# Performance work log

Hardware: AMD Instinct MI355X
Metric: run time of the kernel (lower is better)

Reference implementation:

```python
import jax, jax.numpy as jnp
import numpy as np

B, D, P, C = 256, 2048, 8192, 8
N_CLUSTERS = P // C
MOMENTUM, TEMP = 0.2, 0.07
NEG_INF = jnp.float32(-1e30)


def setup_inputs() -> dict:
    key = jax.random.key(0)
    k1, k2, k3 = jax.random.split(key, 3)
    batch_feat = jax.random.normal(k1, (B, D), dtype=jnp.float32)
    batch_feat = batch_feat / jnp.linalg.norm(batch_feat, axis=1, keepdims=True)
    memory = jax.random.normal(k2, (P, D), dtype=jnp.float32)
    memory = memory / jnp.linalg.norm(memory, axis=1, keepdims=True)
    abs_proxy_label = jax.random.randint(k3, (B,), 0, P, dtype=jnp.int32)
    # each proxy is a (camera, cluster) pair: proxy p -> cam p % C, cluster p // C
    proxy_cam = (jnp.arange(P, dtype=jnp.int32) % C)
    proxy_cluster = (jnp.arange(P, dtype=jnp.int32) // C)
    camid = abs_proxy_label % C               # consistent with mapper[cam]
    pseudo_cluster_label = abs_proxy_label // C
    return dict(batch_feat=batch_feat, memory=memory,
                abs_proxy_label=abs_proxy_label, camid=camid,
                pseudo_cluster_label=pseudo_cluster_label,
                proxy_cam=proxy_cam, proxy_cluster=proxy_cluster,
                epoch=10, inter_loss_epoch=5, k=50)


def reference(batch_feat, memory, abs_proxy_label, camid, pseudo_cluster_label,
              proxy_cam, proxy_cluster, epoch, inter_loss_epoch, k):
    # ---------------- intra-camera proxy loss ----------------
    sim = (batch_feat @ memory.T) / TEMP                      # [B, P]
    cam_mask = camid[:, None] == proxy_cam[None, :]           # per-cam proxy subset
    logits = jnp.where(cam_mask, sim, NEG_INF)
    lse = jax.nn.logsumexp(logits, axis=1)
    tgt = jnp.take_along_axis(logits, abs_proxy_label[:, None].astype(jnp.int32), axis=1)[:, 0]
    ce = lse - tgt                                            # per-sample CE over its cam's proxies
    ones = jnp.ones((B,), dtype=jnp.float32)
    cam_counts = jax.ops.segment_sum(ones, camid, num_segments=C)
    ce_per_cam = jax.ops.segment_sum(ce, camid, num_segments=C)
    intra_loss = jnp.sum(jnp.where(cam_counts > 0, ce_per_cam / jnp.maximum(cam_counts, 1.0), 0.0))

    loss = intra_loss
    # ---------------- inter-camera loss ----------------
    if epoch >= inter_loss_epoch:
        sim_det = jax.lax.stop_gradient(batch_feat) @ memory.T     # kNN uses detached feat, no temp
        pos_mask = (proxy_cluster[None, :] == pseudo_cluster_label[:, None]) & \
                   (proxy_cam[None, :] != camid[:, None])          # same cluster, different cam
        neg_mask = proxy_cluster[None, :] != pseudo_cluster_label[:, None]  # inlier, different cluster
        neg_sim = jnp.where(neg_mask, sim_det, NEG_INF)
        thresh = jax.lax.top_k(neg_sim, k)[0][:, -1]               # drop k nearest negatives
        keep_neg = neg_mask & (sim_det < thresh[:, None])
        full_mask = pos_mask | keep_neg
        inter_logits = jnp.where(full_mask, sim, NEG_INF)
        logsm = inter_logits - jax.nn.logsumexp(inter_logits, axis=1, keepdims=True)
        pos_card = jnp.sum(pos_mask, axis=1).astype(jnp.float32)
        pos_sum = jnp.sum(jnp.where(pos_mask, logsm, 0.0), axis=1)
        loss_i = jnp.where(pos_card > 0, -pos_sum / jnp.maximum(pos_card, 1.0), 0.0)
        inter_per_cam = jax.ops.segment_sum(loss_i, camid, num_segments=C)
        loss = loss + jnp.sum(jnp.where(cam_counts > 0,
                                        0.5 * inter_per_cam / jnp.maximum(cam_counts, 1.0), 0.0))

    # ---------------- EMA memory-bank scatter update (torch does this in backward) ----------------
    def step(mem, xy):
        x, y = xy
        m = MOMENTUM * mem[y] + (1.0 - MOMENTUM) * x
        m = m / jnp.linalg.norm(m)
        return mem.at[y].set(m), None
    new_memory, _ = jax.lax.scan(
        step, memory, (jax.lax.stop_gradient(batch_feat), abs_proxy_label))
    return loss, new_memory
```

## Files before the change

kernel.cpp:

```cpp
#include <hip/hip_runtime.h>
#include <cstdint>

#define NB 256
#define ND 2048
#define NP 8192
#define NEG_INF_F (-1e30f)
#define INV_TEMP (1.0f/0.07f)

typedef __attribute__((ext_vector_type(8))) short          short8;
typedef __attribute__((ext_vector_type(8))) unsigned short ushort8;
typedef __attribute__((ext_vector_type(4))) float          floatx4;

__device__ __forceinline__ unsigned short f2bf(float f) {
  unsigned u = __float_as_uint(f);
  return (unsigned short)((u + 0x7fffu + ((u >> 16) & 1u)) >> 16);
}

__global__ __launch_bounds__(256)
void prep_kernel(const float* __restrict__ mem, const float* __restrict__ feat,
                 unsigned short* __restrict__ Mb, unsigned short* __restrict__ Fb,
                 float* __restrict__ memcopy ) {
  const int b = blockIdx.x, t = threadIdx.x;
  if (b < 8192) {
    const float4* src = (const float4*)(mem + (size_t)b * ND) + 2 * t;
    float4 a = src[0], c = src[1];
    ushort8 r;
    r[0]=f2bf(a.x); r[1]=f2bf(a.y); r[2]=f2bf(a.z); r[3]=f2bf(a.w);
    r[4]=f2bf(c.x); r[5]=f2bf(c.y); r[6]=f2bf(c.z); r[7]=f2bf(c.w);
    *(ushort8*)(Mb + (size_t)b * ND + 8 * t) = r;
    float* dst = memcopy + (size_t)b * ND + 8 * t;
    dst[0]=a.x; dst[1]=a.y; dst[2]=a.z; dst[3]=a.w;
    dst[4]=c.x; dst[5]=c.y; dst[6]=c.z; dst[7]=c.w;
  } else {
    const int i = (b - 8192) * 256 + t;
    const float4* src = (const float4*)feat + 2 * (size_t)i;
    float4 a = src[0], c = src[1];
    ushort8 r;
    r[0]=f2bf(a.x); r[1]=f2bf(a.y); r[2]=f2bf(a.z); r[3]=f2bf(a.w);
    r[4]=f2bf(c.x); r[5]=f2bf(c.y); r[6]=f2bf(c.z); r[7]=f2bf(c.w);
    *(ushort8*)(Fb + 8 * (size_t)i) = r;
  }
}

#define GLOAD_LDS16(g, l) __builtin_amdgcn_global_load_lds( \
  (const __attribute__((address_space(1))) unsigned int*)(g), \
  (__attribute__((address_space(3))) unsigned int*)(l), 16, 0, 0)

__global__ __launch_bounds__(256, 2)
void gemm_kernel(const unsigned short* __restrict__ Fb,
                 const unsigned short* __restrict__ Mb,
                 float* __restrict__ Sout) {
  __shared__ unsigned short sA[2][64 * 64];
  __shared__ unsigned short sB[2][128 * 64];
  const int tid  = threadIdx.x;
  const int wave = tid >> 6;
  const int lane = tid & 63;
  const int frow = lane & 15;
  const int kg   = lane >> 4;
  const int bn0  = blockIdx.x * 128;
  const int bm0  = blockIdx.y * 64;
  const size_t kofs = (size_t)blockIdx.z * 1024;

  const unsigned short* gA[2];
  #pragma unroll
  for (int q = 0; q < 2; ++q) {
    int c = q * 256 + tid, r = c >> 3, kc = (c & 7) ^ (r & 7);
    gA[q] = Fb + (size_t)(bm0 + r) * ND + kofs + kc * 8;
  }
  const unsigned short* gB[4];
  #pragma unroll
  for (int q = 0; q < 4; ++q) {
    int c = q * 256 + tid, r = c >> 3, kc = (c & 7) ^ (r & 7);
    gB[q] = Mb + (size_t)(bn0 + r) * ND + kofs + kc * 8;
  }
  const int ldsb = wave * 512;

  int offA[4][2], offB[2][2];
  #pragma unroll
  for (int m = 0; m < 4; ++m)
    #pragma unroll
    for (int kf = 0; kf < 2; ++kf) {
      int r = m * 16 + frow, sc = (kf * 4 + kg) ^ (r & 7);
      offA[m][kf] = r * 64 + sc * 8;
    }
  #pragma unroll
  for (int n = 0; n < 2; ++n)
    #pragma unroll
    for (int kf = 0; kf < 2; ++kf) {
      int r = wave * 32 + n * 16 + frow, sc = (kf * 4 + kg) ^ (r & 7);
      offB[n][kf] = r * 64 + sc * 8;
    }

  floatx4 acc[4][2];
  #pragma unroll
  for (int m = 0; m < 4; ++m)
    #pragma unroll
    for (int n = 0; n < 2; ++n)
      #pragma unroll
      for (int r = 0; r < 4; ++r) acc[m][n][r] = 0.f;

  auto stage = [&](int buf, int kt) {
    int kk = kt * 64;
    #pragma unroll
    for (int q = 0; q < 2; ++q) GLOAD_LDS16(gA[q] + kk, &sA[buf][q * 2048 + ldsb]);
    #pragma unroll
    for (int q = 0; q < 4; ++q) GLOAD_LDS16(gB[q] + kk, &sB[buf][q * 2048 + ldsb]);
  };
  auto compute = [&](int buf) {
    short8 af[4][2], bf[2][2];
    #pragma unroll
    for (int m = 0; m < 4; ++m)
      #pragma unroll
      for (int kf = 0; kf < 2; ++kf) af[m][kf] = *(const short8*)&sA[buf][offA[m][kf]];
    #pragma unroll
    for (int n = 0; n < 2; ++n)
      #pragma unroll
      for (int kf = 0; kf < 2; ++kf) bf[n][kf] = *(const short8*)&sB[buf][offB[n][kf]];
    #pragma unroll
    for (int m = 0; m < 4; ++m)
      #pragma unroll
      for (int n = 0; n < 2; ++n) {
        acc[m][n] = __builtin_amdgcn_mfma_f32_16x16x32_bf16(af[m][0], bf[n][0], acc[m][n], 0, 0, 0);
        acc[m][n] = __builtin_amdgcn_mfma_f32_16x16x32_bf16(af[m][1], bf[n][1], acc[m][n], 0, 0, 0);
      }
  };

  stage(0, 0);
  __syncthreads();
  int cur = 0;
  for (int kt = 0; kt < 15; ++kt) {
    stage(cur ^ 1, kt + 1);
    compute(cur);
    __syncthreads();
    cur ^= 1;
  }
  compute(cur);

  float* Sp = Sout + (size_t)blockIdx.z * ((size_t)NB * NP);
  #pragma unroll
  for (int m = 0; m < 4; ++m) {
    int row = bm0 + 16 * m + 4 * kg;
    #pragma unroll
    for (int n = 0; n < 2; ++n) {
      int col = bn0 + wave * 32 + 16 * n + frow;
      #pragma unroll
      for (int r = 0; r < 4; ++r)
        Sp[(size_t)(row + r) * NP + col] = acc[m][n][r];
    }
  }
}

__global__ __launch_bounds__(1024)
void row_kernel(const float* __restrict__ S,
                const int* __restrict__ label,
                const int* __restrict__ camid,
                const int* __restrict__ pcl,
                const int* __restrict__ epoch_p,
                const int* __restrict__ ilep_p,
                const int* __restrict__ k_p,
                float* __restrict__ ce_out,
                float* __restrict__ li_out) {
  __shared__ float red[2][16];
  const int i = blockIdx.x, t = threadIdx.x, w = t >> 6;
  const bool l0 = (t & 63) == 0;
  int ph = 0;

  auto bred_sum = [&](float x) -> float {
    #pragma unroll
    for (int o = 32; o; o >>= 1) x += __shfl_xor(x, o);
    if (l0) red[ph][w] = x;
    __syncthreads();
    float s = 0.f;
    #pragma unroll
    for (int q = 0; q < 16; ++q) s += red[ph][q];
    ph ^= 1;
    return s;
  };
  auto bred_max = [&](float x) -> float {
    #pragma unroll
    for (int o = 32; o; o >>= 1) x = fmaxf(x, __shfl_xor(x, o));
    if (l0) red[ph][w] = x;
    __syncthreads();
    float s = NEG_INF_F;
    #pragma unroll
    for (int q = 0; q < 16; ++q) s = fmaxf(s, red[ph][q]);
    ph ^= 1;
    return s;
  };
  auto bred_uni = [&](float x) -> float {
    if (l0) red[ph][w] = x;
    __syncthreads();
    float s = 0.f;
    #pragma unroll
    for (int q = 0; q < 16; ++q) s += red[ph][q];
    ph ^= 1;
    return s;
  };

  const float* r0 = S + (size_t)i * NP;
  const float* r1 = r0 + (size_t)NB * NP;
  float v[8];
  #pragma unroll
  for (int j = 0; j < 8; ++j) v[j] = r0[(j << 10) | t] + r1[(j << 10) | t];

  const int camI = camid[i], clI = pcl[i], lab = label[i];
  const bool myCam = (t & 7) == camI;
  bool neg[8];
  #pragma unroll
  for (int j = 0; j < 8; ++j) neg[j] = (((j << 7) | (t >> 3)) != clI);

  float m1 = NEG_INF_F;
  if (myCam) {
    #pragma unroll
    for (int j = 0; j < 8; ++j) m1 = fmaxf(m1, v[j]);
  }
  m1 = bred_max(m1);
  float s1 = 0.f, tg = 0.f;
  if (myCam) {
    #pragma unroll
    for (int j = 0; j < 8; ++j) s1 += __expf((v[j] - m1) * INV_TEMP);
  }
  #pragma unroll
  for (int j = 0; j < 8; ++j)
    if (((lab >> 10) == j) && (t == (lab & 1023))) tg = v[j];
  s1 = bred_sum(s1);
  tg = bred_sum(tg);
  if (t == 0) ce_out[i] = m1 * INV_TEMP + __logf(s1) - tg * INV_TEMP;

  float li = 0.f;
  if (epoch_p[0] >= ilep_p[0]) {
    const int kneg = k_p[0];
    unsigned kk[8];
    #pragma unroll
    for (int j = 0; j < 8; ++j) {
      unsigned u = __float_as_uint(v[j]);
      kk[j] = (u & 0x80000000u) ? ~u : (u | 0x80000000u);
    }
    unsigned tstar = 0u;
    for (int b = 31; b >= 0; --b) {
      unsigned cand = tstar | (1u << b);
      int cw = 0;
      #pragma unroll
      for (int j = 0; j < 8; ++j)
        cw += __popcll(__ballot(neg[j] && (kk[j] >= cand)));
      float tot = bred_uni((float)cw);
      if (tot >= (float)kneg) tstar = cand;
    }
    float thr = __uint_as_float((tstar & 0x80000000u) ? (tstar ^ 0x80000000u) : ~tstar);

    bool pos[8], keep[8];
    float m2 = NEG_INF_F;
    #pragma unroll
    for (int j = 0; j < 8; ++j) {
      pos[j]  = (!neg[j]) && ((t & 7) != camI);
      keep[j] = neg[j] && (v[j] < thr);
      if (pos[j] || keep[j]) m2 = fmaxf(m2, v[j]);
    }
    m2 = bred_max(m2);
    float s2 = 0.f, sp = 0.f;
    int cw = 0;
    #pragma unroll
    for (int j = 0; j < 8; ++j) {
      if (pos[j] || keep[j]) s2 += __expf((v[j] - m2) * INV_TEMP);
      if (pos[j]) sp += v[j];
      cw += __popcll(__ballot(pos[j]));
    }
    s2 = bred_sum(s2);
    sp = bred_sum(sp);
    float card = bred_uni((float)cw);
    float lse2 = m2 * INV_TEMP + __logf(s2);
    li = (card > 0.f) ? -(sp * INV_TEMP - card * lse2) / card : 0.f;
  }
  if (t == 0) li_out[i] = li;
}

__global__ void finalize_kernel(const float* __restrict__ ce,
                                const float* __restrict__ li,
                                const int* __restrict__ camid,
                                const int* __restrict__ epoch_p,
                                const int* __restrict__ ilep_p,
                                float* __restrict__ out) {
  __shared__ float cnt[8], sa[8], sb[8];
  const int t = threadIdx.x;
  if (t < 8) { cnt[t] = 0.f; sa[t] = 0.f; sb[t] = 0.f; }
  __syncthreads();
  const int c = camid[t];
  atomicAdd(&cnt[c], 1.f);
  atomicAdd(&sa[c], ce[t]);
  atomicAdd(&sb[c], li[t]);
  __syncthreads();
  if (t == 0) {
    const bool inter = epoch_p[0] >= ilep_p[0];
    float l = 0.f;
    for (int q = 0; q < 8; ++q)
      if (cnt[q] > 0.f) {
        l += sa[q] / cnt[q];
        if (inter) l += 0.5f * sb[q] / cnt[q];
      }
    out[0] = l;
  }
}

__global__ __launch_bounds__(256)
void ema_kernel(const float* __restrict__ feat,
                const float* __restrict__ mem,
                const int* __restrict__ label,
                float* __restrict__ outmem) {
  __shared__ float red[4];
  const int b = blockIdx.x, t = threadIdx.x;
  const int y = label[b];
  for (int j = 0; j < b; ++j)
    if (label[j] == y) return;
  float m[8];
  #pragma unroll
  for (int q = 0; q < 8; ++q) m[q] = mem[(size_t)y * ND + q * 256 + t];
  for (int i = b; i < NB; ++i) {
    if (label[i] != y) continue;
    float ss = 0.f;
    #pragma unroll
    for (int q = 0; q < 8; ++q) {
      m[q] = 0.2f * m[q] + 0.8f * feat[(size_t)i * ND + q * 256 + t];
      ss += m[q] * m[q];
    }
    #pragma unroll
    for (int o = 32; o; o >>= 1) ss += __shfl_xor(ss, o);
    if ((t & 63) == 0) red[t >> 6] = ss;
    __syncthreads();
    ss = red[0] + red[1] + red[2] + red[3];
    __syncthreads();
    float inv = 1.f / sqrtf(ss);
    #pragma unroll
    for (int q = 0; q < 8; ++q) m[q] *= inv;
  }
  #pragma unroll
  for (int q = 0; q < 8; ++q) outmem[(size_t)y * ND + q * 256 + t] = m[q];
}

extern "C" void kernel_launch(void* const* d_in, const int* in_sizes, int n_in,
                              void* d_out, int out_size, void* d_ws, size_t ws_size,
                              hipStream_t stream) {
  const float* feat = (const float*)d_in[0];
  const float* mem  = (const float*)d_in[1];
  const int* lab    = (const int*)d_in[2];
  const int* cam    = (const int*)d_in[3];
  const int* pcl    = (const int*)d_in[4];
  const int* ep     = (const int*)d_in[7];
  const int* ilep   = (const int*)d_in[8];
  const int* kp     = (const int*)d_in[9];
  float* out = (float*)d_out;

  char* ws = (char*)d_ws;
  unsigned short* Mb = (unsigned short*)(ws);
  unsigned short* Fb = (unsigned short*)(ws + 33554432);
  float*          S  = (float*)(ws + 34603008);
  float*          ce = (float*)(ws + 51380224);
  float*          li = (float*)(ws + 51381248);

  prep_kernel<<<8448, 256, 0, stream>>>(mem, feat, Mb, Fb, out + 1);
  gemm_kernel<<<dim3(NP / 128, NB / 64, 2), 256, 0, stream>>>(Fb, Mb, S);
  row_kernel<<<NB, 1024, 0, stream>>>(S, lab, cam, pcl, ep, ilep, kp, ce, li);
  finalize_kernel<<<1, 256, 0, stream>>>(ce, li, cam, ep, ilep, out);
  ema_kernel<<<NB, 256, 0, stream>>>(feat, mem, lab, out + 1);
}
```

Baseline: 207.2 us.

## Enlarge GEMM tile to 128x128 with 2x2 wave layout, tidy reductions

The GEMM block tile grows from 64x128 to 128x128. Waves are arranged 2x2, each computing 64x64 with 16 MFMA accumulators, and A and B fragment loads are interleaved per k-slice. This raises arithmetic intensity per LDS/global load but halves the grid to 256 blocks, which lowers occupancy and parallelism on a large-CU device. The row-kernel block reductions now use a shuffle instead of a serial 16-element LDS loop, and the EMA kernel caches labels in shared memory for its duplicate scan.

```diff
diff --git a/kernel.cpp b/kernel.cpp
--- a/kernel.cpp
+++ b/kernel.cpp
@@ -46,83 +46,79 @@
   (const __attribute__((address_space(1))) unsigned int*)(g), \
   (__attribute__((address_space(3))) unsigned int*)(l), 16, 0, 0)
 
-__global__ __launch_bounds__(256, 2)
+__global__ __launch_bounds__(256)
 void gemm_kernel(const unsigned short* __restrict__ Fb,
                  const unsigned short* __restrict__ Mb,
                  float* __restrict__ Sout) {
-  __shared__ unsigned short sA[2][64 * 64];
+  __shared__ unsigned short sA[2][128 * 64];
   __shared__ unsigned short sB[2][128 * 64];
   const int tid  = threadIdx.x;
   const int wave = tid >> 6;
   const int lane = tid & 63;
   const int frow = lane & 15;
   const int kg   = lane >> 4;
+  const int wr   = wave >> 1;
+  const int wc   = wave & 1;
   const int bn0  = blockIdx.x * 128;
-  const int bm0  = blockIdx.y * 64;
+  const int bm0  = blockIdx.y * 128;
   const size_t kofs = (size_t)blockIdx.z * 1024;
 
-  const unsigned short* gA[2];
-  #pragma unroll
-  for (int q = 0; q < 2; ++q) {
+  const unsigned short* gA[4];
+  const unsigned short* gB[4];
+  #pragma unroll
+  for (int q = 0; q < 4; ++q) {
     int c = q * 256 + tid, r = c >> 3, kc = (c & 7) ^ (r & 7);
     gA[q] = Fb + (size_t)(bm0 + r) * ND + kofs + kc * 8;
-  }
-  const unsigned short* gB[4];
-  #pragma unroll
-  for (int q = 0; q < 4; ++q) {
-    int c = q * 256 + tid, r = c >> 3, kc = (c & 7) ^ (r & 7);
     gB[q] = Mb + (size_t)(bn0 + r) * ND + kofs + kc * 8;
   }
   const int ldsb = wave * 512;
 
-  int offA[4][2], offB[2][2];
+  int offA[4][2], offB[4][2];
   #pragma unroll
   for (int m = 0; m < 4; ++m)
     #pragma unroll
     for (int kf = 0; kf < 2; ++kf) {
-      int r = m * 16 + frow, sc = (kf * 4 + kg) ^ (r & 7);
+      int r = wr * 64 + m * 16 + frow, sc = (kf * 4 + kg) ^ (r & 7);
       offA[m][kf] = r * 64 + sc * 8;
     }
   #pragma unroll
-  for (int n = 0; n < 2; ++n)
+  for (int n = 0; n < 4; ++n)
     #pragma unroll
     for (int kf = 0; kf < 2; ++kf) {
-      int r = wave * 32 + n * 16 + frow, sc = (kf * 4 + kg) ^ (r & 7);
+      int r = wc * 64 + n * 16 + frow, sc = (kf * 4 + kg) ^ (r & 7);
       offB[n][kf] = r * 64 + sc * 8;
     }
 
-  floatx4 acc[4][2];
+  floatx4 acc[4][4];
   #pragma unroll
   for (int m = 0; m < 4; ++m)
     #pragma unroll
-    for (int n = 0; n < 2; ++n)
+    for (int n = 0; n < 4; ++n)
       #pragma unroll
       for (int r = 0; r < 4; ++r) acc[m][n][r] = 0.f;
 
   auto stage = [&](int buf, int kt) {
     int kk = kt * 64;
     #pragma unroll
-    for (int q = 0; q < 2; ++q) GLOAD_LDS16(gA[q] + kk, &sA[buf][q * 2048 + ldsb]);
-    #pragma unroll
-    for (int q = 0; q < 4; ++q) GLOAD_LDS16(gB[q] + kk, &sB[buf][q * 2048 + ldsb]);
+    for (int q = 0; q < 4; ++q) {
+      GLOAD_LDS16(gA[q] + kk, &sA[buf][q * 2048 + ldsb]);
+      GLOAD_LDS16(gB[q] + kk, &sB[buf][q * 2048 + ldsb]);
+    }
   };
   auto compute = [&](int buf) {
-    short8 af[4][2], bf[2][2];
-    #pragma unroll
-    for (int m = 0; m < 4; ++m)
-      #pragma unroll
-      for (int kf = 0; kf < 2; ++kf) af[m][kf] = *(const short8*)&sA[buf][offA[m][kf]];
-    #pragma unroll
-    for (int n = 0; n < 2; ++n)
-      #pragma unroll
-      for (int kf = 0; kf < 2; ++kf) bf[n][kf] = *(const short8*)&sB[buf][offB[n][kf]];
-    #pragma unroll
-    for (int m = 0; m < 4; ++m)
-      #pragma unroll
-      for (int n = 0; n < 2; ++n) {
-        acc[m][n] = __builtin_amdgcn_mfma_f32_16x16x32_bf16(af[m][0], bf[n][0], acc[m][n], 0, 0, 0);
-        acc[m][n] = __builtin_amdgcn_mfma_f32_16x16x32_bf16(af[m][1], bf[n][1], acc[m][n], 0, 0, 0);
-      }
+    #pragma unroll
+    for (int kf = 0; kf < 2; ++kf) {
+      short8 af[4], bf[4];
+      #pragma unroll
+      for (int m = 0; m < 4; ++m) af[m] = *(const short8*)&sA[buf][offA[m][kf]];
+      #pragma unroll
+      for (int n = 0; n < 4; ++n) bf[n] = *(const short8*)&sB[buf][offB[n][kf]];
+      #pragma unroll
+      for (int m = 0; m < 4; ++m)
+        #pragma unroll
+        for (int n = 0; n < 4; ++n)
+          acc[m][n] = __builtin_amdgcn_mfma_f32_16x16x32_bf16(af[m], bf[n], acc[m][n], 0, 0, 0);
+    }
   };
 
   stage(0, 0);
@@ -139,10 +135,10 @@
   float* Sp = Sout + (size_t)blockIdx.z * ((size_t)NB * NP);
   #pragma unroll
   for (int m = 0; m < 4; ++m) {
-    int row = bm0 + 16 * m + 4 * kg;
-    #pragma unroll
-    for (int n = 0; n < 2; ++n) {
-      int col = bn0 + wave * 32 + 16 * n + frow;
+    int row = bm0 + wr * 64 + 16 * m + 4 * kg;
+    #pragma unroll
+    for (int n = 0; n < 4; ++n) {
+      int col = bn0 + wc * 64 + 16 * n + frow;
       #pragma unroll
       for (int r = 0; r < 4; ++r)
         Sp[(size_t)(row + r) * NP + col] = acc[m][n][r];
@@ -170,31 +166,31 @@
     for (int o = 32; o; o >>= 1) x += __shfl_xor(x, o);
     if (l0) red[ph][w] = x;
     __syncthreads();
-    float s = 0.f;
-    #pragma unroll
-    for (int q = 0; q < 16; ++q) s += red[ph][q];
+    float r = red[ph][t & 15];
+    #pragma unroll
+    for (int o = 8; o; o >>= 1) r += __shfl_xor(r, o);
     ph ^= 1;
-    return s;
+    return r;
   };
   auto bred_max = [&](float x) -> float {
     #pragma unroll
     for (int o = 32; o; o >>= 1) x = fmaxf(x, __shfl_xor(x, o));
     if (l0) red[ph][w] = x;
     __syncthreads();
-    float s = NEG_INF_F;
-    #pragma unroll
-    for (int q = 0; q < 16; ++q) s = fmaxf(s, red[ph][q]);
+    float r = red[ph][t & 15];
+    #pragma unroll
+    for (int o = 8; o; o >>= 1) r = fmaxf(r, __shfl_xor(r, o));
     ph ^= 1;
-    return s;
+    return r;
   };
   auto bred_uni = [&](float x) -> float {
     if (l0) red[ph][w] = x;
     __syncthreads();
-    float s = 0.f;
-    #pragma unroll
-    for (int q = 0; q < 16; ++q) s += red[ph][q];
+    float r = red[ph][t & 15];
+    #pragma unroll
+    for (int o = 8; o; o >>= 1) r += __shfl_xor(r, o);
     ph ^= 1;
-    return s;
+    return r;
   };
 
   const float* r0 = S + (size_t)i * NP;
@@ -307,15 +303,20 @@
                 const int* __restrict__ label,
                 float* __restrict__ outmem) {
   __shared__ float red[4];
+  __shared__ int slab[NB];
   const int b = blockIdx.x, t = threadIdx.x;
-  const int y = label[b];
+  slab[t] = label[t];
+  __syncthreads();
+  const int y = slab[b];
+  bool mine = true;
   for (int j = 0; j < b; ++j)
-    if (label[j] == y) return;
+    if (slab[j] == y) { mine = false; break; }
+  if (!mine) return;
   float m[8];
   #pragma unroll
   for (int q = 0; q < 8; ++q) m[q] = mem[(size_t)y * ND + q * 256 + t];
   for (int i = b; i < NB; ++i) {
-    if (label[i] != y) continue;
+    if (slab[i] != y) continue;
     float ss = 0.f;
     #pragma unroll
     for (int q = 0; q < 8; ++q) {
@@ -357,7 +358,7 @@
   float*          li = (float*)(ws + 51381248);
 
   prep_kernel<<<8448, 256, 0, stream>>>(mem, feat, Mb, Fb, out + 1);
-  gemm_kernel<<<dim3(NP / 128, NB / 64, 2), 256, 0, stream>>>(Fb, Mb, S);
+  gemm_kernel<<<dim3(NP / 128, NB / 128, 2), 256, 0, stream>>>(Fb, Mb, S);
   row_kernel<<<NB, 1024, 0, stream>>>(S, lab, cam, pcl, ep, ilep, kp, ce, li);
   finalize_kernel<<<1, 256, 0, stream>>>(ce, li, cam, ep, ilep, out);
   ema_kernel<<<NB, 256, 0, stream>>>(feat, mem, lab, out + 1);
```

Result: slower. 217.8 us (+5.1%).

## Fuse finalize into row kernel and radix-4 top-k threshold search

Applied to the files above, without the earlier changes.

The row kernel now uses 512 threads with 16 contiguous elements each, loaded as float4, so each thread holds both camera copies of two clusters. The top-k threshold bit search processes two bits per round with three candidate counts, which halves the number of block reductions. The finalize kernel is removed: per-camera sums are accumulated with atomics and the last block, found via a global counter, computes the loss. The accumulators are zeroed by an extra prep block. The EMA kernel caches labels in shared memory. This cuts launches and reduction barriers, but adds atomics and a last-block pattern that relies on ordering.

```diff
diff --git a/kernel.cpp b/kernel.cpp
--- a/kernel.cpp
+++ b/kernel.cpp
@@ -19,7 +19,8 @@
 __global__ __launch_bounds__(256)
 void prep_kernel(const float* __restrict__ mem, const float* __restrict__ feat,
                  unsigned short* __restrict__ Mb, unsigned short* __restrict__ Fb,
-                 float* __restrict__ memcopy ) {
+                 float* __restrict__ memcopy ,
+                 float* __restrict__ acc, unsigned* __restrict__ counter) {
   const int b = blockIdx.x, t = threadIdx.x;
   if (b < 8192) {
     const float4* src = (const float4*)(mem + (size_t)b * ND) + 2 * t;
@@ -31,7 +32,7 @@
     float* dst = memcopy + (size_t)b * ND + 8 * t;
     dst[0]=a.x; dst[1]=a.y; dst[2]=a.z; dst[3]=a.w;
     dst[4]=c.x; dst[5]=c.y; dst[6]=c.z; dst[7]=c.w;
-  } else {
+  } else if (b < 8448) {
     const int i = (b - 8192) * 256 + t;
     const float4* src = (const float4*)feat + 2 * (size_t)i;
     float4 a = src[0], c = src[1];
@@ -39,6 +40,9 @@
     r[0]=f2bf(a.x); r[1]=f2bf(a.y); r[2]=f2bf(a.z); r[3]=f2bf(a.w);
     r[4]=f2bf(c.x); r[5]=f2bf(c.y); r[6]=f2bf(c.z); r[7]=f2bf(c.w);
     *(ushort8*)(Fb + 8 * (size_t)i) = r;
+  } else {
+    if (t < 16) acc[t] = 0.f;
+    if (t == 16) counter[0] = 0u;
   }
 }
 
@@ -150,7 +154,7 @@
   }
 }
 
-__global__ __launch_bounds__(1024)
+__global__ __launch_bounds__(512)
 void row_kernel(const float* __restrict__ S,
                 const int* __restrict__ label,
                 const int* __restrict__ camid,
@@ -158,146 +162,151 @@
                 const int* __restrict__ epoch_p,
                 const int* __restrict__ ilep_p,
                 const int* __restrict__ k_p,
-                float* __restrict__ ce_out,
-                float* __restrict__ li_out) {
-  __shared__ float red[2][16];
+                float* __restrict__ acc ,
+                unsigned* __restrict__ counter,
+                float* __restrict__ out) {
+  __shared__ float red[2][3][8];
+  __shared__ unsigned sh_done;
+  __shared__ float cnt8[8], gsum[16];
   const int i = blockIdx.x, t = threadIdx.x, w = t >> 6;
   const bool l0 = (t & 63) == 0;
   int ph = 0;
 
-  auto bred_sum = [&](float x) -> float {
-    #pragma unroll
-    for (int o = 32; o; o >>= 1) x += __shfl_xor(x, o);
-    if (l0) red[ph][w] = x;
-    __syncthreads();
-    float s = 0.f;
-    #pragma unroll
-    for (int q = 0; q < 16; ++q) s += red[ph][q];
+  auto bmax = [&](float x) -> float {
+    #pragma unroll
+    for (int o = 32; o; o >>= 1) x = fmaxf(x, __shfl_xor(x, o));
+    if (l0) red[ph][0][w] = x;
+    __syncthreads();
+    float r = red[ph][0][t & 7];
+    #pragma unroll
+    for (int o = 4; o; o >>= 1) r = fmaxf(r, __shfl_xor(r, o));
     ph ^= 1;
-    return s;
-  };
-  auto bred_max = [&](float x) -> float {
-    #pragma unroll
-    for (int o = 32; o; o >>= 1) x = fmaxf(x, __shfl_xor(x, o));
-    if (l0) red[ph][w] = x;
-    __syncthreads();
-    float s = NEG_INF_F;
-    #pragma unroll
-    for (int q = 0; q < 16; ++q) s = fmaxf(s, red[ph][q]);
-    ph ^= 1;
-    return s;
-  };
-  auto bred_uni = [&](float x) -> float {
-    if (l0) red[ph][w] = x;
-    __syncthreads();
-    float s = 0.f;
-    #pragma unroll
-    for (int q = 0; q < 16; ++q) s += red[ph][q];
-    ph ^= 1;
-    return s;
+    return r;
+  };
+  auto bsum2 = [&](float& x, float& y) {
+    #pragma unroll
+    for (int o = 32; o; o >>= 1) { x += __shfl_xor(x, o); y += __shfl_xor(y, o); }
+    if (l0) { red[ph][0][w] = x; red[ph][1][w] = y; }
+    __syncthreads();
+    float rx = red[ph][0][t & 7], ry = red[ph][1][t & 7];
+    #pragma unroll
+    for (int o = 4; o; o >>= 1) { rx += __shfl_xor(rx, o); ry += __shfl_xor(ry, o); }
+    ph ^= 1; x = rx; y = ry;
+  };
+  auto bsum3 = [&](float& x, float& y, float& z) {
+    #pragma unroll
+    for (int o = 32; o; o >>= 1) {
+      x += __shfl_xor(x, o); y += __shfl_xor(y, o); z += __shfl_xor(z, o);
+    }
+    if (l0) { red[ph][0][w] = x; red[ph][1][w] = y; red[ph][2][w] = z; }
+    __syncthreads();
+    float rx = red[ph][0][t & 7], ry = red[ph][1][t & 7], rz = red[ph][2][t & 7];
+    #pragma unroll
+    for (int o = 4; o; o >>= 1) {
+      rx += __shfl_xor(rx, o); ry += __shfl_xor(ry, o); rz += __shfl_xor(rz, o);
+    }
+    ph ^= 1; x = rx; y = ry; z = rz;
   };
 
   const float* r0 = S + (size_t)i * NP;
   const float* r1 = r0 + (size_t)NB * NP;
-  float v[8];
-  #pragma unroll
-  for (int j = 0; j < 8; ++j) v[j] = r0[(j << 10) | t] + r1[(j << 10) | t];
-
+  float v[16];
+  {
+    const float4* a0 = (const float4*)(r0 + (t << 4));
+    const float4* a1 = (const float4*)(r1 + (t << 4));
+    #pragma unroll
+    for (int q = 0; q < 4; ++q) {
+      float4 x = a0[q], y = a1[q];
+      v[4*q+0] = x.x + y.x; v[4*q+1] = x.y + y.y;
+      v[4*q+2] = x.z + y.z; v[4*q+3] = x.w + y.w;
+    }
+  }
   const int camI = camid[i], clI = pcl[i], lab = label[i];
-  const bool myCam = (t & 7) == camI;
-  bool neg[8];
-  #pragma unroll
-  for (int j = 0; j < 8; ++j) neg[j] = (((j << 7) | (t >> 3)) != clI);
-
-  float m1 = NEG_INF_F;
-  if (myCam) {
-    #pragma unroll
-    for (int j = 0; j < 8; ++j) m1 = fmaxf(m1, v[j]);
-  }
-  m1 = bred_max(m1);
-  float s1 = 0.f, tg = 0.f;
-  if (myCam) {
-    #pragma unroll
-    for (int j = 0; j < 8; ++j) s1 += __expf((v[j] - m1) * INV_TEMP);
-  }
-  #pragma unroll
-  for (int j = 0; j < 8; ++j)
-    if (((lab >> 10) == j) && (t == (lab & 1023))) tg = v[j];
-  s1 = bred_sum(s1);
-  tg = bred_sum(tg);
-  if (t == 0) ce_out[i] = m1 * INV_TEMP + __logf(s1) - tg * INV_TEMP;
+  const bool negL = (2 * t)     != clI;
+  const bool negH = (2 * t + 1) != clI;
+
+  float m1 = fmaxf(v[camI], v[camI + 8]);
+  m1 = bmax(m1);
+  float s1 = __expf((v[camI] - m1) * INV_TEMP) + __expf((v[camI + 8] - m1) * INV_TEMP);
+  float tg = (t == (lab >> 4)) ? v[lab & 15] : 0.f;
+  bsum2(s1, tg);
+  const float ce_i = m1 * INV_TEMP + __logf(s1) - tg * INV_TEMP;
 
   float li = 0.f;
-  if (epoch_p[0] >= ilep_p[0]) {
-    const int kneg = k_p[0];
-    unsigned kk[8];
-    #pragma unroll
-    for (int j = 0; j < 8; ++j) {
+  const bool inter = epoch_p[0] >= ilep_p[0];
+  if (inter) {
+    const float kneg = (float)k_p[0];
+    unsigned kk[16];
+    #pragma unroll
+    for (int j = 0; j < 16; ++j) {
       unsigned u = __float_as_uint(v[j]);
       kk[j] = (u & 0x80000000u) ? ~u : (u | 0x80000000u);
     }
     unsigned tstar = 0u;
-    for (int b = 31; b >= 0; --b) {
-      unsigned cand = tstar | (1u << b);
-      int cw = 0;
-      #pragma unroll
-      for (int j = 0; j < 8; ++j)
-        cw += __popcll(__ballot(neg[j] && (kk[j] >= cand)));
-      float tot = bred_uni((float)cw);
-      if (tot >= (float)kneg) tstar = cand;
-    }
-    float thr = __uint_as_float((tstar & 0x80000000u) ? (tstar ^ 0x80000000u) : ~tstar);
-
-    bool pos[8], keep[8];
+    for (int b = 30; b >= 0; b -= 2) {
+      const unsigned c1 = tstar | (1u << b);
+      const unsigned c2 = tstar | (2u << b);
+      const unsigned c3 = tstar | (3u << b);
+      float n1 = 0.f, n2 = 0.f, n3 = 0.f;
+      #pragma unroll
+      for (int j = 0; j < 16; ++j) {
+        const bool ng = (j < 8) ? negL : negH;
+        if (ng) {
+          n1 += (kk[j] >= c1) ? 1.f : 0.f;
+          n2 += (kk[j] >= c2) ? 1.f : 0.f;
+          n3 += (kk[j] >= c3) ? 1.f : 0.f;
+        }
+      }
+      bsum3(n1, n2, n3);
+      if (n2 >= kneg)      tstar = (n3 >= kneg) ? c3 : c2;
+      else if (n1 >= kneg) tstar = c1;
+    }
+    const float thr = __uint_as_float((tstar & 0x80000000u) ? (tstar ^ 0x80000000u) : ~tstar);
+
     float m2 = NEG_INF_F;
-    #pragma unroll
-    for (int j = 0; j < 8; ++j) {
-      pos[j]  = (!neg[j]) && ((t & 7) != camI);
-      keep[j] = neg[j] && (v[j] < thr);
-      if (pos[j] || keep[j]) m2 = fmaxf(m2, v[j]);
-    }
-    m2 = bred_max(m2);
-    float s2 = 0.f, sp = 0.f;
-    int cw = 0;
-    #pragma unroll
-    for (int j = 0; j < 8; ++j) {
-      if (pos[j] || keep[j]) s2 += __expf((v[j] - m2) * INV_TEMP);
-      if (pos[j]) sp += v[j];
-      cw += __popcll(__ballot(pos[j]));
-    }
-    s2 = bred_sum(s2);
-    sp = bred_sum(sp);
-    float card = bred_uni((float)cw);
-    float lse2 = m2 * INV_TEMP + __logf(s2);
+    unsigned posm = 0u, selm = 0u;
+    #pragma unroll
+    for (int j = 0; j < 16; ++j) {
+      const bool ng = (j < 8) ? negL : negH;
+      const bool pos = (!ng) && ((j & 7) != camI);
+      const bool sel = pos || (ng && (v[j] < thr));
+      if (pos) posm |= 1u << j;
+      if (sel) { selm |= 1u << j; m2 = fmaxf(m2, v[j]); }
+    }
+    m2 = bmax(m2);
+    float s2 = 0.f, sp = 0.f, card = 0.f;
+    #pragma unroll
+    for (int j = 0; j < 16; ++j) {
+      if ((selm >> j) & 1u) s2 += __expf((v[j] - m2) * INV_TEMP);
+      if ((posm >> j) & 1u) { sp += v[j]; card += 1.f; }
+    }
+    bsum3(s2, sp, card);
+    const float lse2 = m2 * INV_TEMP + __logf(s2);
     li = (card > 0.f) ? -(sp * INV_TEMP - card * lse2) / card : 0.f;
   }
-  if (t == 0) li_out[i] = li;
-}
-
-__global__ void finalize_kernel(const float* __restrict__ ce,
-                                const float* __restrict__ li,
-                                const int* __restrict__ camid,
-                                const int* __restrict__ epoch_p,
-                                const int* __restrict__ ilep_p,
-                                float* __restrict__ out) {
-  __shared__ float cnt[8], sa[8], sb[8];
-  const int t = threadIdx.x;
-  if (t < 8) { cnt[t] = 0.f; sa[t] = 0.f; sb[t] = 0.f; }
+
+  if (t == 0) {
+    atomicAdd(&acc[camI], ce_i);
+    atomicAdd(&acc[8 + camI], li);
+    __threadfence();
+    sh_done = atomicAdd(counter, 1u);
+  }
   __syncthreads();
-  const int c = camid[t];
-  atomicAdd(&cnt[c], 1.f);
-  atomicAdd(&sa[c], ce[t]);
-  atomicAdd(&sb[c], li[t]);
-  __syncthreads();
-  if (t == 0) {
-    const bool inter = epoch_p[0] >= ilep_p[0];
-    float l = 0.f;
-    for (int q = 0; q < 8; ++q)
-      if (cnt[q] > 0.f) {
-        l += sa[q] / cnt[q];
-        if (inter) l += 0.5f * sb[q] / cnt[q];
-      }
-    out[0] = l;
+  if (sh_done == NB - 1) {
+    if (t < 8) cnt8[t] = 0.f;
+    __syncthreads();
+    if (t < NB) atomicAdd(&cnt8[camid[t]], 1.f);
+    if (t < 16) gsum[t] = acc[t];
+    __syncthreads();
+    if (t == 0) {
+      float l = 0.f;
+      for (int c = 0; c < 8; ++c)
+        if (cnt8[c] > 0.f) {
+          l += gsum[c] / cnt8[c];
+          if (inter) l += 0.5f * gsum[8 + c] / cnt8[c];
+        }
+      out[0] = l;
+    }
   }
 }
 
@@ -307,15 +316,20 @@
                 const int* __restrict__ label,
                 float* __restrict__ outmem) {
   __shared__ float red[4];
+  __shared__ int slab[NB];
   const int b = blockIdx.x, t = threadIdx.x;
-  const int y = label[b];
+  slab[t] = label[t];
+  __syncthreads();
+  const int y = slab[b];
+  bool mine = true;
   for (int j = 0; j < b; ++j)
-    if (label[j] == y) return;
+    if (slab[j] == y) { mine = false; break; }
+  if (!mine) return;
   float m[8];
   #pragma unroll
   for (int q = 0; q < 8; ++q) m[q] = mem[(size_t)y * ND + q * 256 + t];
   for (int i = b; i < NB; ++i) {
-    if (label[i] != y) continue;
+    if (slab[i] != y) continue;
     float ss = 0.f;
     #pragma unroll
     for (int q = 0; q < 8; ++q) {
@@ -353,12 +367,11 @@
   unsigned short* Mb = (unsigned short*)(ws);
   unsigned short* Fb = (unsigned short*)(ws + 33554432);
   float*          S  = (float*)(ws + 34603008);
-  float*          ce = (float*)(ws + 51380224);
-  float*          li = (float*)(ws + 51381248);
-
-  prep_kernel<<<8448, 256, 0, stream>>>(mem, feat, Mb, Fb, out + 1);
+  float*          acc = (float*)(ws + 51380224);
+  unsigned*       ctr = (unsigned*)(ws + 51380224 + 64);
+
+  prep_kernel<<<8449, 256, 0, stream>>>(mem, feat, Mb, Fb, out + 1, acc, ctr);
   gemm_kernel<<<dim3(NP / 128, NB / 64, 2), 256, 0, stream>>>(Fb, Mb, S);
-  row_kernel<<<NB, 1024, 0, stream>>>(S, lab, cam, pcl, ep, ilep, kp, ce, li);
-  finalize_kernel<<<1, 256, 0, stream>>>(ce, li, cam, ep, ilep, out);
+  row_kernel<<<NB, 512, 0, stream>>>(S, lab, cam, pcl, ep, ilep, kp, acc, ctr, out);
   ema_kernel<<<NB, 256, 0, stream>>>(feat, mem, lab, out + 1);
 }
```

New measurement: 219.3 us. 5.8% more time.
